# Kernel tuning notes

Hardware: AMD Instinct MI355X
Metric: run time of the kernel (lower is better)

The kernel has to match this reference:

```python
import jax, jax.numpy as jnp
import numpy as np

B = 32768
D_IN = 512
UNITS = 512


def setup_inputs() -> dict:
    key = jax.random.key(0)
    ks = jax.random.split(key, 12)
    s = 1.0 / np.sqrt(D_IN)
    sh = 1.0 / np.sqrt(UNITS)
    return {
        "inputs": jax.random.normal(ks[0], (B, D_IN), dtype=jnp.float32),
        "state": jax.random.normal(ks[1], (B, UNITS), dtype=jnp.float32),
        "att_score": jax.random.uniform(ks[2], (B, 1), dtype=jnp.float32),
        # update gate
        "Wu_x": jax.random.normal(ks[3], (D_IN, UNITS), dtype=jnp.float32) * s,
        "bu": jnp.zeros((UNITS,), dtype=jnp.float32),
        "Wu_h": jax.random.normal(ks[4], (UNITS, UNITS), dtype=jnp.float32) * sh,
        # reset gate
        "Wr_x": jax.random.normal(ks[5], (D_IN, UNITS), dtype=jnp.float32) * s,
        "br": jnp.zeros((UNITS,), dtype=jnp.float32),
        "Wr_h": jax.random.normal(ks[6], (UNITS, UNITS), dtype=jnp.float32) * sh,
        # candidate memory
        "Wc_x": jax.random.normal(ks[7], (D_IN, UNITS), dtype=jnp.float32) * s,
        "bc": jnp.zeros((UNITS,), dtype=jnp.float32),
        "Wc_h": jax.random.normal(ks[8], (UNITS, UNITS), dtype=jnp.float32) * sh,
    }


def reference(inputs, state, att_score, Wu_x, bu, Wu_h, Wr_x, br, Wr_h, Wc_x, bc, Wc_h):
    # u = sigmoid(Dense_act(x) + Dense_noact(h))
    u = jax.nn.sigmoid(inputs @ Wu_x + bu + state @ Wu_h)
    # r = sigmoid(Dense_act(x) + Dense_noact(h))
    r = jax.nn.sigmoid(inputs @ Wr_x + br + state @ Wr_h)
    # c = tanh(Dense_act(x) + r * Dense_noact(h))
    c = jnp.tanh(inputs @ Wc_x + bc + r * (state @ Wc_h))
    u_ = att_score * u  # [B,1] * [B,U] broadcast
    state_next = (1.0 - u_) * state + u_ * c
    return state_next
```

## Files before the change

### kernel.cpp

```cpp
#include <hip/hip_runtime.h>
#include <hip/hip_bf16.h>
#include <stdint.h>

#define B_ROWS 32768
#define DIM 512
#define THREADS 512
#define NKT 32
#define ABUF 8192
#define WBUF 12288
#define BUF (ABUF + WBUF)

typedef __attribute__((ext_vector_type(8))) __bf16 bf16x8;
typedef __attribute__((ext_vector_type(4))) float f32x4;
typedef __attribute__((ext_vector_type(4))) unsigned int uint4v;

__device__ static inline unsigned short f2bf(float f) {
    unsigned int u = __builtin_bit_cast(unsigned int, f);
    u += 0x7fffu + ((u >> 16) & 1u);
    return (unsigned short)(u >> 16);
}

__device__ static inline void load_lds_16B(const void* g, void* lds) {
    __builtin_amdgcn_global_load_lds(
        (const __attribute__((address_space(1))) unsigned int*)g,
        (__attribute__((address_space(3))) unsigned int*)lds,
        16, 0, 0);
}

__global__ void prep_weights(const float* __restrict__ Wu_x, const float* __restrict__ Wu_h,
                             const float* __restrict__ Wr_x, const float* __restrict__ Wr_h,
                             const float* __restrict__ Wc_x, const float* __restrict__ Wc_h,
                             unsigned short* __restrict__ Wt2) {
    __shared__ float tile[32][33];
    const int t = blockIdx.z;
    const int k0 = blockIdx.x * 32;
    const int n0 = blockIdx.y * 32;
    const float* Wx = (t == 0) ? Wu_x : (t == 1) ? Wr_x : Wc_x;
    const float* Wh = (t == 0) ? Wu_h : (t == 1) ? Wr_h : Wc_h;
    const int tid = threadIdx.x;
    const int c = tid & 31, r0 = tid >> 5;
#pragma unroll
    for (int i = 0; i < 4; ++i) {
        int kl = r0 + i * 8;
        int k = k0 + kl;
        int n = n0 + c;
        float v = (k < 512) ? Wx[(size_t)k * 512 + n] : Wh[(size_t)(k - 512) * 512 + n];
        tile[kl][c] = v;
    }
    __syncthreads();
    const int kt = k0 >> 5;
#pragma unroll
    for (int i = 0; i < 4; ++i) {
        int nl = r0 + i * 8;
        int kc = c;
        int n = n0 + nl;
        size_t base = (((size_t)kt * 3 + t) * 512 + n) * 64;
        *(unsigned short*)((char*)Wt2 + base + ((kc * 2) ^ (((n >> 1) & 3) << 4))) =
            f2bf(tile[kc][nl]);
    }
}

__global__ __launch_bounds__(512) void prep_A(const float* __restrict__ x,
                                              const float* __restrict__ h,
                                              unsigned short* __restrict__ Apack) {
    const size_t i = (size_t)blockIdx.x * 512 + threadIdx.x;
    const int slot = (int)(i & 3);
    const int row = (int)((i >> 2) & 32767);
    const int kt = (int)(i >> 17);
    const int k0 = kt * 32 + slot * 8;
    const float* src = (k0 < 512) ? (x + (size_t)row * 512 + k0)
                                  : (h + (size_t)row * 512 + (k0 - 512));
    float4 f0 = *(const float4*)(src + 0);
    float4 f1 = *(const float4*)(src + 4);
    uint4v p;
    p.x = f2bf(f0.x) | ((unsigned)f2bf(f0.y) << 16);
    p.y = f2bf(f0.z) | ((unsigned)f2bf(f0.w) << 16);
    p.z = f2bf(f1.x) | ((unsigned)f2bf(f1.y) << 16);
    p.w = f2bf(f1.z) | ((unsigned)f2bf(f1.w) << 16);
    char* dst = (char*)Apack + (((size_t)kt << 15) + row) * 64
              + ((slot * 16) ^ (((row >> 1) & 3) << 4));
    *(uint4v*)dst = p;
}

__global__ __launch_bounds__(THREADS, 4) void augru_main(
    const float* __restrict__ h, const float* __restrict__ att,
    const unsigned short* __restrict__ Wt2, const unsigned short* __restrict__ Apack,
    const float* __restrict__ bu, const float* __restrict__ br,
    const float* __restrict__ bc, float* __restrict__ out) {
    extern __shared__ char smem[];
    const int tid = threadIdx.x;
    const int lane = tid & 63;
    const int wid = tid >> 6;
    const int wm = wid >> 2;
    const int wn = wid & 3;
    const int id = blockIdx.x;
    const int wg = (id & 7) * 256 + (id >> 3);
    const int nb = wg & 7;
    const int mb = wg >> 3;
    const int cl = lane & 15;
    const int kg = lane >> 4;

    f32x4 accU[4], accR[4], accCx[4], accCh[4];
#pragma unroll
    for (int i = 0; i < 4; ++i) {
        accU[i] = (f32x4)(0.f);
        accR[i] = (f32x4)(0.f);
        accCx[i] = (f32x4)(0.f);
        accCh[i] = (f32x4)(0.f);
    }

    auto stage = [&](int buf, int kt) {
        const char* gA = (const char*)Apack + (((size_t)kt << 15) + (size_t)mb * 128) * 64;
        load_lds_16B(gA + tid * 16, smem + buf * BUF + wid * 1024);
        {
            const int b = tid * 16;
            const int t = b >> 12;
            const int off = b & 4095;
            const char* gW = (const char*)Wt2
                + (((size_t)kt * 3 + t) * 512 + nb * 64) * 64 + off;
            load_lds_16B(gW, smem + buf * BUF + ABUF + wid * 1024);
        }
        if (wid < 4) {
            const char* gW = (const char*)Wt2
                + (((size_t)kt * 3 + 2) * 512 + nb * 64) * 64 + tid * 16;
            load_lds_16B(gW, smem + buf * BUF + ABUF + 8192 + wid * 1024);
        }
    };

    stage(0, 0);
    __syncthreads();

    auto body = [&](int kt, f32x4(&accC)[4]) {
        const int buf = kt & 1;
        if (kt + 1 < NKT) stage(buf ^ 1, kt + 1);
        const char* aB = smem + buf * BUF;
        const char* wB = aB + ABUF;
        bf16x8 a[4], bb[3];
#pragma unroll
        for (int mi = 0; mi < 4; ++mi) {
            const int row = wm * 64 + mi * 16 + cl;
            a[mi] = __builtin_bit_cast(
                bf16x8, *(const uint4v*)(aB + row * 64
                    + ((kg * 16) ^ (((row >> 1) & 3) << 4))));
        }
        const int col = wn * 16 + cl;
#pragma unroll
        for (int t = 0; t < 3; ++t)
            bb[t] = __builtin_bit_cast(
                bf16x8, *(const uint4v*)(wB + t * 4096 + col * 64
                    + ((kg * 16) ^ (((col >> 1) & 3) << 4))));
        __builtin_amdgcn_s_setprio(1);
#pragma unroll
        for (int mi = 0; mi < 4; ++mi)
            accU[mi] = __builtin_amdgcn_mfma_f32_16x16x32_bf16(
                a[mi], bb[0], accU[mi], 0, 0, 0);
#pragma unroll
        for (int mi = 0; mi < 4; ++mi)
            accR[mi] = __builtin_amdgcn_mfma_f32_16x16x32_bf16(
                a[mi], bb[1], accR[mi], 0, 0, 0);
#pragma unroll
        for (int mi = 0; mi < 4; ++mi)
            accC[mi] = __builtin_amdgcn_mfma_f32_16x16x32_bf16(
                a[mi], bb[2], accC[mi], 0, 0, 0);
        __builtin_amdgcn_s_setprio(0);
        __syncthreads();
    };

    for (int kt = 0; kt < 16; ++kt) body(kt, accCx);
    for (int kt = 16; kt < 32; ++kt) body(kt, accCh);

    {
        const int col = nb * 64 + wn * 16 + cl;
        const float bU = bu[col];
        const float bR = br[col];
        const float bC = bc[col];
#pragma unroll
        for (int mi = 0; mi < 4; ++mi) {
#pragma unroll
            for (int j = 0; j < 4; ++j) {
                const int row = mb * 128 + wm * 64 + mi * 16 + kg * 4 + j;
                const float up = accU[mi][j] + bU;
                const float rp = accR[mi][j] + bR;
                const float u = 1.f / (1.f + __expf(-up));
                const float r = 1.f / (1.f + __expf(-rp));
                const float cpre = accCx[mi][j] + bC + r * accCh[mi][j];
                const float e = __expf(-2.f * cpre);
                const float cc = (1.f - e) / (1.f + e);
                const float aa = att[row];
                const float hv = h[(size_t)row * 512 + col];
                const float u_ = aa * u;
                out[(size_t)row * 512 + col] = (1.f - u_) * hv + u_ * cc;
            }
        }
    }
}

extern "C" void kernel_launch(void* const* d_in, const int* in_sizes, int n_in,
                              void* d_out, int out_size, void* d_ws, size_t ws_size,
                              hipStream_t stream) {
    const float* x    = (const float*)d_in[0];
    const float* h    = (const float*)d_in[1];
    const float* att  = (const float*)d_in[2];
    const float* Wu_x = (const float*)d_in[3];
    const float* bu   = (const float*)d_in[4];
    const float* Wu_h = (const float*)d_in[5];
    const float* Wr_x = (const float*)d_in[6];
    const float* br   = (const float*)d_in[7];
    const float* Wr_h = (const float*)d_in[8];
    const float* Wc_x = (const float*)d_in[9];
    const float* bc   = (const float*)d_in[10];
    const float* Wc_h = (const float*)d_in[11];
    unsigned short* Wt2 = (unsigned short*)d_ws;
    unsigned short* Apack = (unsigned short*)((char*)d_ws + (4 << 20));
    float* out = (float*)d_out;

    prep_weights<<<dim3(32, 16, 3), 256, 0, stream>>>(Wu_x, Wu_h, Wr_x, Wr_h, Wc_x, Wc_h, Wt2);
    prep_A<<<dim3(8192), 512, 0, stream>>>(x, h, Apack);

    hipFuncSetAttribute((const void*)augru_main,
                        hipFuncAttributeMaxDynamicSharedMemorySize, 2 * BUF);
    augru_main<<<dim3(2048), THREADS, 2 * BUF, stream>>>(
        h, att, Wt2, Apack, bu, br, bc, out);
}
```

Baseline: 149.2 us.

## Triple-buffer LDS staging with vmcnt waits and a single barrier per k-step

Moves the GEMM main loop from double to triple buffering: two stages are prefetched ahead. Explicit s_waitcnt vmcnt plus one s_barrier per iteration replace the two __syncthreads. Load issue is reorganised so waves 0-3 fetch the three weight tiles and waves 4-7 fetch the A tile. LDS per block grows from 40KB to 60KB, which may reduce how many blocks fit on a CU and makes the per-wave load counts uneven.

```diff
diff --git a/kernel.cpp b/kernel.cpp
--- a/kernel.cpp
+++ b/kernel.cpp
@@ -110,30 +110,35 @@
     }
 
     auto stage = [&](int buf, int kt) {
-        const char* gA = (const char*)Apack + (((size_t)kt << 15) + (size_t)mb * 128) * 64;
-        load_lds_16B(gA + tid * 16, smem + buf * BUF + wid * 1024);
-        {
-            const int b = tid * 16;
-            const int t = b >> 12;
-            const int off = b & 4095;
-            const char* gW = (const char*)Wt2
-                + (((size_t)kt * 3 + t) * 512 + nb * 64) * 64 + off;
-            load_lds_16B(gW, smem + buf * BUF + ABUF + wid * 1024);
-        }
+        char* base = smem + buf * BUF;
         if (wid < 4) {
-            const char* gW = (const char*)Wt2
-                + (((size_t)kt * 3 + 2) * 512 + nb * 64) * 64 + tid * 16;
-            load_lds_16B(gW, smem + buf * BUF + ABUF + 8192 + wid * 1024);
+            const int i = tid * 16;
+#pragma unroll
+            for (int t = 0; t < 3; ++t) {
+                const char* gW = (const char*)Wt2
+                    + (((size_t)kt * 3 + t) * 512 + nb * 64) * 64;
+                load_lds_16B(gW + i, base + ABUF + t * 4096 + wid * 1024);
+            }
+        } else {
+            const int i = (tid - 256) * 16;
+            const char* gA = (const char*)Apack
+                + (((size_t)kt << 15) + (size_t)mb * 128) * 64;
+            load_lds_16B(gA + i, base + (wid - 4) * 1024);
+            load_lds_16B(gA + 4096 + i, base + 4096 + (wid - 4) * 1024);
         }
     };
 
     stage(0, 0);
-    __syncthreads();
+    stage(1, 1);
 
     auto body = [&](int kt, f32x4(&accC)[4]) {
-        const int buf = kt & 1;
-        if (kt + 1 < NKT) stage(buf ^ 1, kt + 1);
-        const char* aB = smem + buf * BUF;
+        if (kt == NKT - 1)
+            asm volatile("s_waitcnt vmcnt(0)" ::: "memory");
+        else
+            asm volatile("s_waitcnt vmcnt(2)" ::: "memory");
+        __builtin_amdgcn_s_barrier();
+        if (kt + 2 < NKT) stage((kt + 2) % 3, kt + 2);
+        const char* aB = smem + (kt % 3) * BUF;
         const char* wB = aB + ABUF;
         bf16x8 a[4], bb[3];
 #pragma unroll
@@ -163,7 +168,6 @@
             accC[mi] = __builtin_amdgcn_mfma_f32_16x16x32_bf16(
                 a[mi], bb[2], accC[mi], 0, 0, 0);
         __builtin_amdgcn_s_setprio(0);
-        __syncthreads();
     };
 
     for (int kt = 0; kt < 16; ++kt) body(kt, accCx);
@@ -218,7 +222,7 @@
     prep_A<<<dim3(8192), 512, 0, stream>>>(x, h, Apack);
 
     hipFuncSetAttribute((const void*)augru_main,
-                        hipFuncAttributeMaxDynamicSharedMemorySize, 2 * BUF);
-    augru_main<<<dim3(2048), THREADS, 2 * BUF, stream>>>(
+                        hipFuncAttributeMaxDynamicSharedMemorySize, 3 * BUF);
+    augru_main<<<dim3(2048), THREADS, 3 * BUF, stream>>>(
         h, att, Wt2, Apack, bu, br, bc, out);
 }
```

New measurement: 146.7 us. About the same (-1.7%).

## Double K-tile depth to 64 and split staging loads across warp groups

Applied to the files above, without the earlier changes.

Raises the K step per pipeline stage from 32 to 64, which halves the number of barrier-separated iterations and doubles the LDS buffers. The packed A and weight layouts change to 128-byte rows with a matching XOR swizzle. Global-to-LDS staging is now split by role: four waves load weights and four load activations. The end-of-iteration __syncthreads is replaced by vmcnt wait plus s_barrier at the start of each iteration, and LDS offsets are precomputed. The larger LDS footprint (80KB) may cut the number of resident blocks per CU.

```diff
diff --git a/kernel.cpp b/kernel.cpp
--- a/kernel.cpp
+++ b/kernel.cpp
@@ -5,9 +5,9 @@
 #define B_ROWS 32768
 #define DIM 512
 #define THREADS 512
-#define NKT 32
-#define ABUF 8192
-#define WBUF 12288
+#define NKT 16
+#define ABUF 16384
+#define WBUF 24576
 #define BUF (ABUF + WBUF)
 
 typedef __attribute__((ext_vector_type(8))) __bf16 bf16x8;
@@ -48,14 +48,15 @@
         tile[kl][c] = v;
     }
     __syncthreads();
-    const int kt = k0 >> 5;
+    const int kt = k0 >> 6;
+    const int kkb = k0 & 32;
 #pragma unroll
     for (int i = 0; i < 4; ++i) {
         int nl = r0 + i * 8;
         int kc = c;
         int n = n0 + nl;
-        size_t base = (((size_t)kt * 3 + t) * 512 + n) * 64;
-        *(unsigned short*)((char*)Wt2 + base + ((kc * 2) ^ (((n >> 1) & 3) << 4))) =
+        size_t base = (((size_t)kt * 3 + t) * 512 + n) * 128;
+        *(unsigned short*)((char*)Wt2 + base + (((kkb + kc) * 2) ^ ((n & 7) << 4))) =
             f2bf(tile[kc][nl]);
     }
 }
@@ -64,10 +65,10 @@
                                               const float* __restrict__ h,
                                               unsigned short* __restrict__ Apack) {
     const size_t i = (size_t)blockIdx.x * 512 + threadIdx.x;
-    const int slot = (int)(i & 3);
-    const int row = (int)((i >> 2) & 32767);
-    const int kt = (int)(i >> 17);
-    const int k0 = kt * 32 + slot * 8;
+    const int s = (int)(i & 7);
+    const int row = (int)((i >> 3) & 32767);
+    const int kt = (int)(i >> 18);
+    const int k0 = kt * 64 + s * 8;
     const float* src = (k0 < 512) ? (x + (size_t)row * 512 + k0)
                                   : (h + (size_t)row * 512 + (k0 - 512));
     float4 f0 = *(const float4*)(src + 0);
@@ -77,8 +78,8 @@
     p.y = f2bf(f0.z) | ((unsigned)f2bf(f0.w) << 16);
     p.z = f2bf(f1.x) | ((unsigned)f2bf(f1.y) << 16);
     p.w = f2bf(f1.z) | ((unsigned)f2bf(f1.w) << 16);
-    char* dst = (char*)Apack + (((size_t)kt << 15) + row) * 64
-              + ((slot * 16) ^ (((row >> 1) & 3) << 4));
+    char* dst = (char*)Apack + (((size_t)kt * 32768 + row) * 128)
+              + ((s * 16) ^ ((row & 7) << 4));
     *(uint4v*)dst = p;
 }
 
@@ -109,65 +110,82 @@
         accCh[i] = (f32x4)(0.f);
     }
 
+    const int swz = (cl & 7) << 4;
+    int aOff[2][4], wOff[2][3];
+#pragma unroll
+    for (int ks = 0; ks < 2; ++ks) {
+        const int kbyte = ks * 64 + kg * 16;
+#pragma unroll
+        for (int mi = 0; mi < 4; ++mi)
+            aOff[ks][mi] = (wm * 64 + mi * 16 + cl) * 128 + (kbyte ^ swz);
+#pragma unroll
+        for (int t = 0; t < 3; ++t)
+            wOff[ks][t] = ABUF + t * 8192 + (wn * 16 + cl) * 128 + (kbyte ^ swz);
+    }
+
+    const char* gWbase = (const char*)Wt2 + (size_t)nb * 8192;
+    const char* gAbase = (const char*)Apack + (size_t)mb * 128 * 128;
     auto stage = [&](int buf, int kt) {
-        const char* gA = (const char*)Apack + (((size_t)kt << 15) + (size_t)mb * 128) * 64;
-        load_lds_16B(gA + tid * 16, smem + buf * BUF + wid * 1024);
-        {
-            const int b = tid * 16;
-            const int t = b >> 12;
-            const int off = b & 4095;
-            const char* gW = (const char*)Wt2
-                + (((size_t)kt * 3 + t) * 512 + nb * 64) * 64 + off;
-            load_lds_16B(gW, smem + buf * BUF + ABUF + wid * 1024);
-        }
+        char* base = smem + buf * BUF;
         if (wid < 4) {
-            const char* gW = (const char*)Wt2
-                + (((size_t)kt * 3 + 2) * 512 + nb * 64) * 64 + tid * 16;
-            load_lds_16B(gW, smem + buf * BUF + ABUF + 8192 + wid * 1024);
+            const char* gW = gWbase + (size_t)kt * (3 * 512 * 128);
+#pragma unroll
+            for (int q = 0; q < 6; ++q) {
+                const int b = wid * 6144 + q * 1024 + lane * 16;
+                const int t = b >> 13;
+                load_lds_16B(gW + t * 57344 + b, base + ABUF + (b & ~1023));
+            }
+        } else {
+            const char* gA = gAbase + (size_t)kt * (32768 * 128);
+#pragma unroll
+            for (int q = 0; q < 4; ++q) {
+                const int b = (wid - 4) * 4096 + q * 1024 + lane * 16;
+                load_lds_16B(gA + b, base + (b & ~1023));
+            }
         }
     };
 
     stage(0, 0);
-    __syncthreads();
-
-    auto body = [&](int kt, f32x4(&accC)[4]) {
-        const int buf = kt & 1;
+
+    auto body = [&](int kt, int buf, f32x4(&accC)[4]) {
+        asm volatile("s_waitcnt vmcnt(0)" ::: "memory");
+        __builtin_amdgcn_s_barrier();
         if (kt + 1 < NKT) stage(buf ^ 1, kt + 1);
         const char* aB = smem + buf * BUF;
-        const char* wB = aB + ABUF;
-        bf16x8 a[4], bb[3];
-#pragma unroll
-        for (int mi = 0; mi < 4; ++mi) {
-            const int row = wm * 64 + mi * 16 + cl;
-            a[mi] = __builtin_bit_cast(
-                bf16x8, *(const uint4v*)(aB + row * 64
-                    + ((kg * 16) ^ (((row >> 1) & 3) << 4))));
+#pragma unroll
+        for (int ks = 0; ks < 2; ++ks) {
+            bf16x8 a[4], bb[3];
+#pragma unroll
+            for (int mi = 0; mi < 4; ++mi)
+                a[mi] = __builtin_bit_cast(bf16x8, *(const uint4v*)(aB + aOff[ks][mi]));
+#pragma unroll
+            for (int t = 0; t < 3; ++t)
+                bb[t] = __builtin_bit_cast(bf16x8, *(const uint4v*)(aB + wOff[ks][t]));
+            __builtin_amdgcn_s_setprio(1);
+#pragma unroll
+            for (int mi = 0; mi < 4; ++mi)
+                accU[mi] = __builtin_amdgcn_mfma_f32_16x16x32_bf16(
+                    a[mi], bb[0], accU[mi], 0, 0, 0);
+#pragma unroll
+            for (int mi = 0; mi < 4; ++mi)
+                accR[mi] = __builtin_amdgcn_mfma_f32_16x16x32_bf16(
+                    a[mi], bb[1], accR[mi], 0, 0, 0);
+#pragma unroll
+            for (int mi = 0; mi < 4; ++mi)
+                accC[mi] = __builtin_amdgcn_mfma_f32_16x16x32_bf16(
+                    a[mi], bb[2], accC[mi], 0, 0, 0);
+            __builtin_amdgcn_s_setprio(0);
         }
-        const int col = wn * 16 + cl;
-#pragma unroll
-        for (int t = 0; t < 3; ++t)
-            bb[t] = __builtin_bit_cast(
-                bf16x8, *(const uint4v*)(wB + t * 4096 + col * 64
-                    + ((kg * 16) ^ (((col >> 1) & 3) << 4))));
-        __builtin_amdgcn_s_setprio(1);
-#pragma unroll
-        for (int mi = 0; mi < 4; ++mi)
-            accU[mi] = __builtin_amdgcn_mfma_f32_16x16x32_bf16(
-                a[mi], bb[0], accU[mi], 0, 0, 0);
-#pragma unroll
-        for (int mi = 0; mi < 4; ++mi)
-            accR[mi] = __builtin_amdgcn_mfma_f32_16x16x32_bf16(
-                a[mi], bb[1], accR[mi], 0, 0, 0);
-#pragma unroll
-        for (int mi = 0; mi < 4; ++mi)
-            accC[mi] = __builtin_amdgcn_mfma_f32_16x16x32_bf16(
-                a[mi], bb[2], accC[mi], 0, 0, 0);
-        __builtin_amdgcn_s_setprio(0);
-        __syncthreads();
     };
 
-    for (int kt = 0; kt < 16; ++kt) body(kt, accCx);
-    for (int kt = 16; kt < 32; ++kt) body(kt, accCh);
+    for (int kp = 0; kp < 4; ++kp) {
+        body(kp * 2, 0, accCx);
+        body(kp * 2 + 1, 1, accCx);
+    }
+    for (int kp = 4; kp < 8; ++kp) {
+        body(kp * 2, 0, accCh);
+        body(kp * 2 + 1, 1, accCh);
+    }
 
     {
         const int col = nb * 64 + wn * 16 + cl;
```

Result: slower. 277.6 us (+86.1%).
